# Optimization experiments

Hardware: AMD Instinct MI355X
Metric: run time of the kernel (lower is better)

## Reference

```python
import jax, jax.numpy as jnp
import numpy as np

D_MODEL = 512
NUM_HEADS = 8
HEAD_DIM = D_MODEL // NUM_HEADS


def setup_inputs() -> dict:
    key = jax.random.key(0)
    ks = jax.random.split(key, 12)
    B, S, D = 4, 2048, D_MODEL
    s = 1.0 / np.sqrt(D)
    return {
        "x": jax.random.normal(ks[0], (B, S, D), dtype=jnp.float32),
        "timestamps": jax.random.uniform(ks[1], (B, S), dtype=jnp.float32),
        "attention_mask": jnp.ones((B, S), dtype=jnp.int32),
        "Wq": jax.random.normal(ks[2], (D, D), dtype=jnp.float32) * s,
        "bq": jnp.zeros((D,), dtype=jnp.float32),
        "Wk": jax.random.normal(ks[3], (D, D), dtype=jnp.float32) * s,
        "bk": jnp.zeros((D,), dtype=jnp.float32),
        "Wv": jax.random.normal(ks[4], (D, D), dtype=jnp.float32) * s,
        "bv": jnp.zeros((D,), dtype=jnp.float32),
        "Wo": jax.random.normal(ks[5], (D, D), dtype=jnp.float32) * s,
        "bo": jnp.zeros((D,), dtype=jnp.float32),
        "decay_lambda": jnp.ones((NUM_HEADS,), dtype=jnp.float32),
    }


def reference(x, timestamps, attention_mask, Wq, bq, Wk, bk, Wv, bv, Wo, bo, decay_lambda):
    B, S, D = x.shape
    H, hd = NUM_HEADS, HEAD_DIM
    scale = hd ** -0.5
    q = (x @ Wq + bq).reshape(B, S, H, hd)
    k = (x @ Wk + bk).reshape(B, S, H, hd)
    v = (x @ Wv + bv).reshape(B, S, H, hd)
    # [B,H,S,S] raw scores
    scores = jnp.einsum("bihd,bjhd->bhij", q, k) * scale
    # learnable exponential time decay, multiplied into scores
    time_diff_abs = jnp.abs(timestamps[:, :, None] - timestamps[:, None, :])  # [B,S,S]
    lam = jax.nn.softplus(decay_lambda)  # [H]
    decay_bias = jnp.exp(-lam[None, :, None, None] * time_diff_abs[:, None])  # [B,H,S,S]
    scores = scores * decay_bias
    # mask over key positions
    scores = jnp.where(attention_mask[:, None, None, :] == 0, -jnp.inf, scores)
    attn = jax.nn.softmax(scores, axis=-1)
    out = jnp.einsum("bhij,bjhd->bihd", attn, v).reshape(B, S, D)
    out = out @ Wo + bo
    return out, attn
```

## Files before the change

kernel.cpp:

```cpp
#include <hip/hip_runtime.h>


#define S_LEN  2048
#define DM     512
#define NH     8
#define HDIM   64
#define BATCH  4
#define BHN    32
#define BSROWS 8192

typedef __attribute__((ext_vector_type(8))) short short8v;
typedef __attribute__((ext_vector_type(8))) unsigned short ushort8v;
typedef __attribute__((ext_vector_type(4))) unsigned short ushort4v;
typedef __attribute__((ext_vector_type(4))) float f32x4;
typedef __attribute__((ext_vector_type(2))) unsigned int uint2v;

static __device__ __forceinline__ unsigned short bf16_rne(float f){
  unsigned int u = __float_as_uint(f);
  u = (u + 0x7FFFu + ((u >> 16) & 1u)) >> 16;
  return (unsigned short)u;
}
static __device__ __forceinline__ float bf16_f32(unsigned short h){
  return __uint_as_float(((unsigned int)h) << 16);
}
static __device__ __forceinline__ unsigned int pack2bf(float a, float b){
  return (unsigned int)bf16_rne(a) | ((unsigned int)bf16_rne(b) << 16);
}
static __device__ __forceinline__ f32x4 mfma16(short8v a, short8v b, f32x4 c){
  return __builtin_amdgcn_mfma_f32_16x16x32_bf16(a, b, c, 0, 0, 0);
}
static __device__ __forceinline__ void gll16(const unsigned short* g, unsigned short* l){
  __builtin_amdgcn_global_load_lds(
      (const __attribute__((address_space(1))) unsigned int*)g,
      (__attribute__((address_space(3))) unsigned int*)l, 16, 0, 0);
}

__global__ void k_split(const float* __restrict__ src,
                        unsigned short* __restrict__ hi,
                        unsigned short* __restrict__ lo, int n){
  for (int i = blockIdx.x*blockDim.x + threadIdx.x; i < n;
       i += gridDim.x*blockDim.x){
    float f = src[i];
    unsigned short h = bf16_rne(f);
    hi[i] = h;
    lo[i] = bf16_rne(f - bf16_f32(h));
  }
}

__global__ void k_wsplit(const float* __restrict__ W,
                         unsigned short* __restrict__ Thi,
                         unsigned short* __restrict__ Tlo){
  int idx = blockIdx.x*blockDim.x + threadIdx.x;
  int n = idx >> 9, k = idx & 511;
  float f = W[k*DM + n];
  unsigned short h = bf16_rne(f);
  Thi[idx] = h;
  Tlo[idx] = bf16_rne(f - bf16_f32(h));
}

__global__ __launch_bounds__(256, 3) void k_gemm_split(
    const unsigned short* __restrict__ Ahi, const unsigned short* __restrict__ Alo,
    const unsigned short* __restrict__ BThi, const unsigned short* __restrict__ BTlo,
    const float* __restrict__ bias,
    float* __restrict__ outF,
    unsigned short* __restrict__ outHi, unsigned short* __restrict__ outLo,
    int M, int N, int K, int mode, float cscale)
{
  __shared__ __align__(16) unsigned short At[2][2][128][32];
  __shared__ __align__(16) unsigned short Bt[2][2][64][32];
  const int lane = threadIdx.x & 63, w = threadIdx.x >> 6;
  const int lr = lane & 15, lk = lane >> 4;
  const int rowbase = blockIdx.y*128;
  const int colbase = blockIdx.x*64;
  const int wrow = (w >> 1)*64;
  const int wcol = (w & 1)*32;

  const int srow = w*16 + (lane>>2);
  const int ssw  = ((lane&3) ^ ((lane>>3)&3))*8;
  const unsigned short* asrc_h = Ahi + (size_t)(rowbase + srow)*K + ssw;
  const unsigned short* asrc_l = Alo + (size_t)(rowbase + srow)*K + ssw;
  const unsigned short* bsrc_h = BThi + (size_t)(colbase + srow)*K + ssw;
  const unsigned short* bsrc_l = BTlo + (size_t)(colbase + srow)*K + ssw;
  unsigned short* adst_h = &At[0][0][w*16][0];
  unsigned short* adst_l = &At[0][1][w*16][0];
  unsigned short* bdst_h = &Bt[0][0][w*16][0];
  unsigned short* bdst_l = &Bt[0][1][w*16][0];

#define GSTAGE(KS, BB) { \
    int k0_ = (KS)*32; \
    gll16(asrc_h + k0_,              adst_h + (BB)*8192); \
    gll16(asrc_h + (size_t)64*K + k0_, adst_h + (BB)*8192 + 2048); \
    gll16(asrc_l + k0_,              adst_l + (BB)*8192); \
    gll16(asrc_l + (size_t)64*K + k0_, adst_l + (BB)*8192 + 2048); \
    gll16(bsrc_h + k0_,              bdst_h + (BB)*4096); \
    gll16(bsrc_l + k0_,              bdst_l + (BB)*4096); }

  const int csw = (lk ^ ((lr>>1)&3))*8;
  const unsigned short* Ard_h = &At[0][0][wrow + lr][0] + csw;
  const unsigned short* Ard_l = &At[0][1][wrow + lr][0] + csw;
  const unsigned short* Brd_h = &Bt[0][0][wcol + lr][0] + csw;
  const unsigned short* Brd_l = &Bt[0][1][wcol + lr][0] + csw;

  f32x4 acc[4][2];
#pragma unroll
  for (int mi=0; mi<4; ++mi)
#pragma unroll
    for (int ni=0; ni<2; ++ni) acc[mi][ni] = (f32x4){0.f,0.f,0.f,0.f};

  GSTAGE(0, 0);
  __syncthreads();

  const int NKS = K >> 5;
  for (int ks = 0; ks < NKS; ++ks){
    const int c = ks & 1;
    if (ks + 1 < NKS) GSTAGE(ks+1, c^1);
    short8v ah[4], al[4], bhf[2], blf[2];
#pragma unroll
    for (int mi=0; mi<4; ++mi){
      ah[mi] = *(const short8v*)(Ard_h + c*8192 + mi*512);
      al[mi] = *(const short8v*)(Ard_l + c*8192 + mi*512);
    }
#pragma unroll
    for (int ni=0; ni<2; ++ni){
      bhf[ni] = *(const short8v*)(Brd_h + c*4096 + ni*512);
      blf[ni] = *(const short8v*)(Brd_l + c*4096 + ni*512);
    }
#pragma unroll
    for (int mi=0; mi<4; ++mi)
#pragma unroll
      for (int ni=0; ni<2; ++ni){
        acc[mi][ni] = mfma16(ah[mi], blf[ni], acc[mi][ni]);
        acc[mi][ni] = mfma16(al[mi], bhf[ni], acc[mi][ni]);
        acc[mi][ni] = mfma16(ah[mi], bhf[ni], acc[mi][ni]);
      }
    __syncthreads();
  }
#undef GSTAGE

#pragma unroll
  for (int mi=0; mi<4; ++mi)
#pragma unroll
    for (int ni=0; ni<2; ++ni){
      const int col = colbase + wcol + ni*16 + lr;
      const int row0 = rowbase + wrow + mi*16 + lk*4;
      if (mode == 1){
        int b = row0 >> 11, s0 = row0 & 2047, hh = col >> 6, d = col & 63;
        ushort4v t;
#pragma unroll
        for (int r=0;r<4;++r)
          t[r] = bf16_rne((acc[mi][ni][r] + bias[col]) * cscale);
        *(ushort4v*)(outHi + ((size_t)(b*NH + hh)*HDIM + d)*S_LEN + s0) = t;
      } else {
#pragma unroll
        for (int r=0;r<4;++r){
          int row = row0 + r;
          float cvl = (acc[mi][ni][r] + bias[col]) * cscale;
          if (mode == 2){
            outF[(size_t)row*N + col] = cvl;
          } else {
            int b = row >> 11, s = row & 2047, hh = col >> 6, d = col & 63;
            size_t off = (((size_t)(b*NH + hh))*S_LEN + s)*HDIM + d;
            unsigned short hb = bf16_rne(cvl);
            outHi[off] = hb;
            outLo[off] = bf16_rne(cvl - bf16_f32(hb));
          }
        }
      }
    }
}

__global__ __launch_bounds__(256) void k_rowsum(
    const unsigned short* __restrict__ qhi,
    const unsigned short* __restrict__ khi,
    const float* __restrict__ ts, const int* __restrict__ am,
    const float* __restrict__ dlam,
    float* __restrict__ rs_part)
{
  __shared__ __align__(16) unsigned short K_t[2][32][64];
  __shared__ __align__(16) float ts_l[1024];
  __shared__ __align__(16) float mb_l[1024];
  const int w = threadIdx.x >> 6, lane = threadIdx.x & 63;
  const int lr = lane & 15, lk = lane >> 4;
  const int wg = blockIdx.x;
  const int sw = (wg & 7)*256 + (wg >> 3);
  const int bh = sw >> 6, rem = sw & 63, it = rem >> 1, jh = rem & 1;
  const int b = bh >> 3, h = bh & 7;
  const int i0 = it*64 + w*16;
  const int j0 = jh*1024;

  const float* tsb = ts + b*S_LEN;
  const int*   amb = am + b*S_LEN;
  for (int i = threadIdx.x; i < 1024; i += 256){
    ts_l[i] = tsb[j0+i];
    mb_l[i] = amb[j0+i] ? 0.f : -1e30f;
  }

  float nlam2 = -log1pf(expf(dlam[h])) * 1.44269504f;
  nlam2 = __uint_as_float(__builtin_amdgcn_readfirstlane(__float_as_uint(nlam2)));

  size_t qoff = ((size_t)bh*S_LEN + i0 + lr)*HDIM + lk*8;
  const short8v qh0 = *(const short8v*)(qhi + qoff);
  const short8v qh1 = *(const short8v*)(qhi + qoff + 32);
  const float ti = tsb[i0 + lr];

  const unsigned short* kbh = khi + ((size_t)bh*S_LEN + j0)*HDIM;
  const unsigned short* ksrc = kbh + ((lane>>3))*64
                             + (((lane&7)^((lane>>3)&7))*8) + w*512;
  unsigned short* kdst = &K_t[0][0][0] + w*512;

  gll16(ksrc, kdst);
  __syncthreads();

  float rs = 0.f;
  for (int t = 0; t < 32; ++t){
    const int c = t & 1;
    if (t < 31) gll16(ksrc + (t+1)*2048, kdst + (c^1)*2048);
#pragma unroll
    for (int s = 0; s < 2; ++s){
      const unsigned short* Kr = &K_t[c][s*16 + lr][0];
      short8v a0 = *(const short8v*)(Kr + ((lk ^ (lr&7))*8));
      short8v a1 = *(const short8v*)(Kr + (((4+lk) ^ (lr&7))*8));
      f32x4 sA = (f32x4){0.f,0.f,0.f,0.f};
      sA = mfma16(a0, qh0, sA);
      sA = mfma16(a1, qh1, sA);
      const int jb = t*32 + s*16 + lk*4;
      f32x4 ts4 = *(const f32x4*)&ts_l[jb];
      f32x4 mb4 = *(const f32x4*)&mb_l[jb];
#pragma unroll
      for (int r=0;r<4;++r){
        float dec = __builtin_amdgcn_exp2f(nlam2 * fabsf(ti - ts4[r]));
        rs += __builtin_amdgcn_exp2f(__builtin_fmaf(sA[r], dec, mb4[r]));
      }
    }
    __syncthreads();
  }
  rs += __shfl_xor(rs, 16, 64);
  rs += __shfl_xor(rs, 32, 64);
  if (lane < 16)
    rs_part[(size_t)(jh*BHN + bh)*S_LEN + i0 + lane] = rs;
}

__global__ __launch_bounds__(256, 4) void k_pass2(
    const unsigned short* __restrict__ qhi, const unsigned short* __restrict__ qlo,
    const unsigned short* __restrict__ khi, const unsigned short* __restrict__ klo,
    const unsigned short* __restrict__ vT,
    const float* __restrict__ ts, const int* __restrict__ am,
    const float* __restrict__ dlam,
    const float* __restrict__ rs_part,
    float* __restrict__ attn,
    unsigned short* __restrict__ p0hi, unsigned short* __restrict__ p0lo,
    unsigned short* __restrict__ p1hi, unsigned short* __restrict__ p1lo)
{
  __shared__ __align__(16) unsigned short K_t[2][2][32][64];
  __shared__ __align__(16) unsigned short V_t[2][64][32];
  __shared__ __align__(16) float ts_l[1024];
  __shared__ __align__(16) float mb_l[1024];
  __shared__ __align__(16) unsigned int pb[4][16][20];
  const int w = threadIdx.x >> 6, lane = threadIdx.x & 63;
  const int lr = lane & 15, lk = lane >> 4;
  const int wg = blockIdx.x;
  const int sw = (wg & 7)*256 + (wg >> 3);
  const int bh = sw >> 6, rem = sw & 63, it = rem >> 1, jh = rem & 1;
  const int b = bh >> 3, h = bh & 7;
  const int i0 = it*64 + w*16;
  const int j0 = jh*1024;

  const float* tsb = ts + b*S_LEN;
  const int*   amb = am + b*S_LEN;
  for (int i = threadIdx.x; i < 1024; i += 256){
    ts_l[i] = tsb[j0+i];
    mb_l[i] = amb[j0+i] ? 0.f : -1e30f;
  }

  float nlam2 = -log1pf(expf(dlam[h])) * 1.44269504f;
  nlam2 = __uint_as_float(__builtin_amdgcn_readfirstlane(__float_as_uint(nlam2)));

  size_t qoff = ((size_t)bh*S_LEN + i0 + lr)*HDIM + lk*8;
  const short8v qh0 = *(const short8v*)(qhi + qoff);
  const short8v qh1 = *(const short8v*)(qhi + qoff + 32);
  const short8v ql0 = *(const short8v*)(qlo + qoff);
  const short8v ql1 = *(const short8v*)(qlo + qoff + 32);
  const float ti = tsb[i0 + lr];

  float tot = rs_part[(size_t)bh*S_LEN + i0 + lr]
            + rs_part[(size_t)(BHN + bh)*S_LEN + i0 + lr];
  const float rinv = tot > 0.f ? 1.f/tot : 0.f;

  const unsigned short* kbh = khi + ((size_t)bh*S_LEN + j0)*HDIM;
  const unsigned short* kbl = klo + ((size_t)bh*S_LEN + j0)*HDIM;
  const unsigned short* vtb = vT + (size_t)bh*HDIM*S_LEN;
  unsigned int* pbw = &pb[w][0][0];

  const int ksw = ((lane&7)^((lane>>3)&7))*8;
  const unsigned short* ksrc_h = kbh + (lane>>3)*64 + ksw + w*512;
  const unsigned short* ksrc_l = kbl + (lane>>3)*64 + ksw + w*512;
  const unsigned short* vsrc = vtb + ((size_t)(w*16 + (lane>>2)))*S_LEN + j0
                             + (((lane&3)^((lane>>4)&3))*8);
  unsigned short* kdst_h = &K_t[0][0][0][0] + w*512;
  unsigned short* kdst_l = &K_t[0][1][0][0] + w*512;
  unsigned short* vdst   = &V_t[0][0][0]    + w*512;

  const unsigned int abase = (unsigned int)(bh*S_LEN + i0 + lr)*S_LEN + j0;

  gll16(ksrc_h, kdst_h);
  gll16(ksrc_l, kdst_l);
  gll16(vsrc,   vdst);
  __syncthreads();

  f32x4 oaccT0 = (f32x4){0.f,0.f,0.f,0.f};
  f32x4 oaccT1 = (f32x4){0.f,0.f,0.f,0.f};
  f32x4 oaccT2 = (f32x4){0.f,0.f,0.f,0.f};
  f32x4 oaccT3 = (f32x4){0.f,0.f,0.f,0.f};

  for (int t = 0; t < 32; ++t){
    const int c = t & 1;
    if (t < 31){
      gll16(ksrc_h + (t+1)*2048, kdst_h + (c^1)*4096);
      gll16(ksrc_l + (t+1)*2048, kdst_l + (c^1)*4096);
      gll16(vsrc   + (t+1)*32,   vdst   + (c^1)*2048);
    }
#pragma unroll
    for (int s = 0; s < 2; ++s){
      const unsigned short* Kr0 = &K_t[c][0][s*16 + lr][0];
      const unsigned short* Kr1 = &K_t[c][1][s*16 + lr][0];
      short8v kh0 = *(const short8v*)(Kr0 + ((lk ^ (lr&7))*8));
      short8v kh1 = *(const short8v*)(Kr0 + (((4+lk) ^ (lr&7))*8));
      short8v kl0 = *(const short8v*)(Kr1 + ((lk ^ (lr&7))*8));
      short8v kl1 = *(const short8v*)(Kr1 + (((4+lk) ^ (lr&7))*8));
      f32x4 s1 = (f32x4){0.f,0.f,0.f,0.f};
      s1 = mfma16(kh0, ql0, s1);
      s1 = mfma16(kl0, qh0, s1);
      s1 = mfma16(kh1, ql1, s1);
      s1 = mfma16(kl1, qh1, s1);
      f32x4 s2 = (f32x4){0.f,0.f,0.f,0.f};
      s2 = mfma16(kh0, qh0, s2);
      s2 = mfma16(kh1, qh1, s2);
      const int jb = t*32 + s*16 + lk*4;
      f32x4 ts4 = *(const f32x4*)&ts_l[jb];
      f32x4 mb4 = *(const f32x4*)&mb_l[jb];
      f32x4 pv;
#pragma unroll
      for (int r=0;r<4;++r){
        float sa = s1[r] + s2[r];
        float dec = __builtin_amdgcn_exp2f(nlam2 * fabsf(ti - ts4[r]));
        float e = __builtin_amdgcn_exp2f(__builtin_fmaf(sa, dec, mb4[r]));
        pv[r] = e * rinv;
      }
      *(f32x4*)(attn + abase + jb) = pv;
      uint2v pk; pk.x = pack2bf(pv[0], pv[1]); pk.y = pack2bf(pv[2], pv[3]);
      *(uint2v*)&pbw[lr*20 + s*8 + 2*lk] = pk;
    }
    short8v pa = *(const short8v*)&pbw[lr*20 + 4*lk];
    const int vsw = (lr>>2)&3;
    short8v vf0 = *(const short8v*)&V_t[c][ 0 + lr][(lk ^ vsw)*8];
    short8v vf1 = *(const short8v*)&V_t[c][16 + lr][(lk ^ vsw)*8];
    short8v vf2 = *(const short8v*)&V_t[c][32 + lr][(lk ^ vsw)*8];
    short8v vf3 = *(const short8v*)&V_t[c][48 + lr][(lk ^ vsw)*8];
    oaccT0 = mfma16(vf0, pa, oaccT0);
    oaccT1 = mfma16(vf1, pa, oaccT1);
    oaccT2 = mfma16(vf2, pa, oaccT2);
    oaccT3 = mfma16(vf3, pa, oaccT3);
    __syncthreads();
  }

  unsigned short* phi = jh ? p1hi : p0hi;
  unsigned short* plo = jh ? p1lo : p0lo;
  const size_t rowb = (size_t)(b*S_LEN + i0 + lr)*DM + h*HDIM + lk*4;
  float oa[4][4] = {
    {oaccT0[0],oaccT0[1],oaccT0[2],oaccT0[3]},
    {oaccT1[0],oaccT1[1],oaccT1[2],oaccT1[3]},
    {oaccT2[0],oaccT2[1],oaccT2[2],oaccT2[3]},
    {oaccT3[0],oaccT3[1],oaccT3[2],oaccT3[3]}};
#pragma unroll
  for (int nt=0;nt<4;++nt){
    ushort4v hh, ll;
#pragma unroll
    for (int r=0;r<4;++r){
      float vv = oa[nt][r];
      unsigned short hb = bf16_rne(vv);
      hh[r] = hb;
      ll[r] = bf16_rne(vv - bf16_f32(hb));
    }
    *(ushort4v*)(phi + rowb + nt*16) = hh;
    *(ushort4v*)(plo + rowb + nt*16) = ll;
  }
}

__global__ __launch_bounds__(256) void k_combine(
    const unsigned short* __restrict__ h1, const unsigned short* __restrict__ l1,
    unsigned short* __restrict__ oh, unsigned short* __restrict__ ol, int n8)
{
  int i = blockIdx.x*blockDim.x + threadIdx.x;
  if (i >= n8) return;
  size_t base = (size_t)i*8;
  ushort8v a = *(const ushort8v*)(oh + base);
  ushort8v bq = *(const ushort8v*)(ol + base);
  ushort8v c = *(const ushort8v*)(h1 + base);
  ushort8v d = *(const ushort8v*)(l1 + base);
  ushort8v rh, rl;
#pragma unroll
  for (int j=0;j<8;++j){
    float f = bf16_f32(a[j]) + bf16_f32(bq[j]) + bf16_f32(c[j]) + bf16_f32(d[j]);
    unsigned short hb = bf16_rne(f);
    rh[j] = hb;
    rl[j] = bf16_rne(f - bf16_f32(hb));
  }
  *(ushort8v*)(oh + base) = rh;
  *(ushort8v*)(ol + base) = rl;
}

extern "C" void kernel_launch(void* const* d_in, const int* in_sizes, int n_in,
                              void* d_out, int out_size, void* d_ws, size_t ws_size,
                              hipStream_t stream){
  const float* x  = (const float*)d_in[0];
  const float* ts = (const float*)d_in[1];
  const int*   am = (const int*)d_in[2];
  const float* Wq = (const float*)d_in[3];
  const float* bq = (const float*)d_in[4];
  const float* Wk = (const float*)d_in[5];
  const float* bk = (const float*)d_in[6];
  const float* Wv = (const float*)d_in[7];
  const float* bv = (const float*)d_in[8];
  const float* Wo = (const float*)d_in[9];
  const float* bo = (const float*)d_in[10];
  const float* dl = (const float*)d_in[11];

  char* ws = (char*)d_ws;
  unsigned short* xhi = (unsigned short*)(ws);
  unsigned short* xlo = (unsigned short*)(ws + 8388608ull);
  unsigned short* wqt_hi = (unsigned short*)(ws + 16777216ull + 0ull*524288ull);
  unsigned short* wqt_lo = (unsigned short*)(ws + 16777216ull + 1ull*524288ull);
  unsigned short* wkt_hi = (unsigned short*)(ws + 16777216ull + 2ull*524288ull);
  unsigned short* wkt_lo = (unsigned short*)(ws + 16777216ull + 3ull*524288ull);
  unsigned short* wvt_hi = (unsigned short*)(ws + 16777216ull + 4ull*524288ull);
  unsigned short* wvt_lo = (unsigned short*)(ws + 16777216ull + 5ull*524288ull);
  unsigned short* wot_hi = (unsigned short*)(ws + 16777216ull + 6ull*524288ull);
  unsigned short* wot_lo = (unsigned short*)(ws + 16777216ull + 7ull*524288ull);
  unsigned short* qhi = (unsigned short*)(ws + 20971520ull + 0ull*8388608ull);
  unsigned short* qlo = (unsigned short*)(ws + 20971520ull + 1ull*8388608ull);
  unsigned short* khi = (unsigned short*)(ws + 20971520ull + 2ull*8388608ull);
  unsigned short* klo = (unsigned short*)(ws + 20971520ull + 3ull*8388608ull);
  unsigned short* vt  = (unsigned short*)(ws + 20971520ull + 4ull*8388608ull);
  float* rs_part = (float*)(ws + 16777216ull);

  float* outp  = (float*)d_out;
  float* attnp = outp + (size_t)BSROWS*DM;
  unsigned short* p1hi = (unsigned short*)d_out;
  unsigned short* p1lo = p1hi + 4194304ull;

  k_split<<<4096, 256, 0, stream>>>(x, xhi, xlo, BSROWS*DM);
  k_wsplit<<<1024, 256, 0, stream>>>(Wq, wqt_hi, wqt_lo);
  k_wsplit<<<1024, 256, 0, stream>>>(Wk, wkt_hi, wkt_lo);
  k_wsplit<<<1024, 256, 0, stream>>>(Wv, wvt_hi, wvt_lo);
  k_wsplit<<<1024, 256, 0, stream>>>(Wo, wot_hi, wot_lo);

  dim3 pg(DM/64, BSROWS/128);
  k_gemm_split<<<pg, 256, 0, stream>>>(xhi, xlo, wqt_hi, wqt_lo, bq,
                                       nullptr, qhi, qlo, BSROWS, DM, DM, 0,
                                       0.18033688f);
  k_gemm_split<<<pg, 256, 0, stream>>>(xhi, xlo, wkt_hi, wkt_lo, bk,
                                       nullptr, khi, klo, BSROWS, DM, DM, 0, 1.f);
  k_gemm_split<<<pg, 256, 0, stream>>>(xhi, xlo, wvt_hi, wvt_lo, bv,
                                       nullptr, vt, nullptr, BSROWS, DM, DM, 1, 1.f);

  k_rowsum<<<2048, 256, 0, stream>>>(qhi, khi, ts, am, dl, rs_part);
  k_pass2<<<2048, 256, 0, stream>>>(qhi, qlo, khi, klo, vt, ts, am, dl,
                                    rs_part, attnp, xhi, xlo, p1hi, p1lo);
  k_combine<<<2048, 256, 0, stream>>>(p1hi, p1lo, xhi, xlo, 524288);
  k_gemm_split<<<pg, 256, 0, stream>>>(xhi, xlo, wot_hi, wot_lo, bo,
                                       outp, nullptr, nullptr, BSROWS, DM, DM, 2, 1.f);

  (void)in_sizes; (void)n_in; (void)out_size; (void)ws_size;
}
```

Baseline: 399.6 us.

## Widen projection GEMM tile to 128x128 and fuse weight-split launches

The split-bf16 GEMM block tile grows from 128x64 to 128x128, so each wave computes a 64x64 sub-tile with a 4x4 accumulator array. The staging loads and LDS B-buffer are resized to match, and the occupancy hint is dropped from the launch bounds. This raises reuse of the A operand per LDS load and halves the block count, at the cost of higher register and LDS use per block. Separately, the four weight transpose/split kernels are merged into one launch to cut launch overhead.

New measurement: 418.6 us. 4.7% more time.

```diff
diff --git a/kernel.cpp b/kernel.cpp
--- a/kernel.cpp
+++ b/kernel.cpp
@@ -47,18 +47,28 @@
   }
 }
 
-__global__ void k_wsplit(const float* __restrict__ W,
-                         unsigned short* __restrict__ Thi,
-                         unsigned short* __restrict__ Tlo){
+__global__ void k_wsplit4(
+    const float* __restrict__ Wq, const float* __restrict__ Wk,
+    const float* __restrict__ Wv, const float* __restrict__ Wo,
+    unsigned short* __restrict__ qh, unsigned short* __restrict__ ql,
+    unsigned short* __restrict__ kh, unsigned short* __restrict__ kl,
+    unsigned short* __restrict__ vh, unsigned short* __restrict__ vl,
+    unsigned short* __restrict__ oh, unsigned short* __restrict__ ol)
+{
   int idx = blockIdx.x*blockDim.x + threadIdx.x;
-  int n = idx >> 9, k = idx & 511;
+  int wsel = idx >> 18;
+  int off  = idx & 262143;
+  int n = off >> 9, k = off & 511;
+  const float* W = wsel==0 ? Wq : wsel==1 ? Wk : wsel==2 ? Wv : Wo;
+  unsigned short* H = wsel==0 ? qh : wsel==1 ? kh : wsel==2 ? vh : oh;
+  unsigned short* L = wsel==0 ? ql : wsel==1 ? kl : wsel==2 ? vl : ol;
   float f = W[k*DM + n];
   unsigned short h = bf16_rne(f);
-  Thi[idx] = h;
-  Tlo[idx] = bf16_rne(f - bf16_f32(h));
-}
-
-__global__ __launch_bounds__(256, 3) void k_gemm_split(
+  H[off] = h;
+  L[off] = bf16_rne(f - bf16_f32(h));
+}
+
+__global__ __launch_bounds__(256) void k_gemm_split(
     const unsigned short* __restrict__ Ahi, const unsigned short* __restrict__ Alo,
     const unsigned short* __restrict__ BThi, const unsigned short* __restrict__ BTlo,
     const float* __restrict__ bias,
@@ -67,33 +77,35 @@
     int M, int N, int K, int mode, float cscale)
 {
   __shared__ __align__(16) unsigned short At[2][2][128][32];
-  __shared__ __align__(16) unsigned short Bt[2][2][64][32];
+  __shared__ __align__(16) unsigned short Bt[2][2][128][32];
   const int lane = threadIdx.x & 63, w = threadIdx.x >> 6;
   const int lr = lane & 15, lk = lane >> 4;
   const int rowbase = blockIdx.y*128;
-  const int colbase = blockIdx.x*64;
+  const int colbase = blockIdx.x*128;
   const int wrow = (w >> 1)*64;
-  const int wcol = (w & 1)*32;
-
-  const int srow = w*16 + (lane>>2);
+  const int wcol = (w & 1)*64;
+
+  const int srow = w*32 + (lane>>2);
   const int ssw  = ((lane&3) ^ ((lane>>3)&3))*8;
-  const unsigned short* asrc_h = Ahi + (size_t)(rowbase + srow)*K + ssw;
-  const unsigned short* asrc_l = Alo + (size_t)(rowbase + srow)*K + ssw;
+  const unsigned short* asrc_h = Ahi  + (size_t)(rowbase + srow)*K + ssw;
+  const unsigned short* asrc_l = Alo  + (size_t)(rowbase + srow)*K + ssw;
   const unsigned short* bsrc_h = BThi + (size_t)(colbase + srow)*K + ssw;
   const unsigned short* bsrc_l = BTlo + (size_t)(colbase + srow)*K + ssw;
-  unsigned short* adst_h = &At[0][0][w*16][0];
-  unsigned short* adst_l = &At[0][1][w*16][0];
-  unsigned short* bdst_h = &Bt[0][0][w*16][0];
-  unsigned short* bdst_l = &Bt[0][1][w*16][0];
+  unsigned short* adst_h = &At[0][0][w*32][0];
+  unsigned short* adst_l = &At[0][1][w*32][0];
+  unsigned short* bdst_h = &Bt[0][0][w*32][0];
+  unsigned short* bdst_l = &Bt[0][1][w*32][0];
 
 #define GSTAGE(KS, BB) { \
     int k0_ = (KS)*32; \
-    gll16(asrc_h + k0_,              adst_h + (BB)*8192); \
-    gll16(asrc_h + (size_t)64*K + k0_, adst_h + (BB)*8192 + 2048); \
-    gll16(asrc_l + k0_,              adst_l + (BB)*8192); \
-    gll16(asrc_l + (size_t)64*K + k0_, adst_l + (BB)*8192 + 2048); \
-    gll16(bsrc_h + k0_,              bdst_h + (BB)*4096); \
-    gll16(bsrc_l + k0_,              bdst_l + (BB)*4096); }
+    gll16(asrc_h + k0_,                adst_h + (BB)*8192); \
+    gll16(asrc_h + (size_t)16*K + k0_, adst_h + (BB)*8192 + 512); \
+    gll16(asrc_l + k0_,                adst_l + (BB)*8192); \
+    gll16(asrc_l + (size_t)16*K + k0_, adst_l + (BB)*8192 + 512); \
+    gll16(bsrc_h + k0_,                bdst_h + (BB)*8192); \
+    gll16(bsrc_h + (size_t)16*K + k0_, bdst_h + (BB)*8192 + 512); \
+    gll16(bsrc_l + k0_,                bdst_l + (BB)*8192); \
+    gll16(bsrc_l + (size_t)16*K + k0_, bdst_l + (BB)*8192 + 512); }
 
   const int csw = (lk ^ ((lr>>1)&3))*8;
   const unsigned short* Ard_h = &At[0][0][wrow + lr][0] + csw;
@@ -101,11 +113,11 @@
   const unsigned short* Brd_h = &Bt[0][0][wcol + lr][0] + csw;
   const unsigned short* Brd_l = &Bt[0][1][wcol + lr][0] + csw;
 
-  f32x4 acc[4][2];
+  f32x4 acc[4][4];
 #pragma unroll
   for (int mi=0; mi<4; ++mi)
 #pragma unroll
-    for (int ni=0; ni<2; ++ni) acc[mi][ni] = (f32x4){0.f,0.f,0.f,0.f};
+    for (int ni=0; ni<4; ++ni) acc[mi][ni] = (f32x4){0.f,0.f,0.f,0.f};
 
   GSTAGE(0, 0);
   __syncthreads();
@@ -114,21 +126,21 @@
   for (int ks = 0; ks < NKS; ++ks){
     const int c = ks & 1;
     if (ks + 1 < NKS) GSTAGE(ks+1, c^1);
-    short8v ah[4], al[4], bhf[2], blf[2];
+    short8v ah[4], al[4], bhf[4], blf[4];
 #pragma unroll
     for (int mi=0; mi<4; ++mi){
       ah[mi] = *(const short8v*)(Ard_h + c*8192 + mi*512);
       al[mi] = *(const short8v*)(Ard_l + c*8192 + mi*512);
     }
 #pragma unroll
-    for (int ni=0; ni<2; ++ni){
-      bhf[ni] = *(const short8v*)(Brd_h + c*4096 + ni*512);
-      blf[ni] = *(const short8v*)(Brd_l + c*4096 + ni*512);
+    for (int ni=0; ni<4; ++ni){
+      bhf[ni] = *(const short8v*)(Brd_h + c*8192 + ni*512);
+      blf[ni] = *(const short8v*)(Brd_l + c*8192 + ni*512);
     }
 #pragma unroll
     for (int mi=0; mi<4; ++mi)
 #pragma unroll
-      for (int ni=0; ni<2; ++ni){
+      for (int ni=0; ni<4; ++ni){
         acc[mi][ni] = mfma16(ah[mi], blf[ni], acc[mi][ni]);
         acc[mi][ni] = mfma16(al[mi], bhf[ni], acc[mi][ni]);
         acc[mi][ni] = mfma16(ah[mi], bhf[ni], acc[mi][ni]);
@@ -140,7 +152,7 @@
 #pragma unroll
   for (int mi=0; mi<4; ++mi)
 #pragma unroll
-    for (int ni=0; ni<2; ++ni){
+    for (int ni=0; ni<4; ++ni){
       const int col = colbase + wcol + ni*16 + lr;
       const int row0 = rowbase + wrow + mi*16 + lk*4;
       if (mode == 1){
@@ -449,12 +461,11 @@
   unsigned short* p1lo = p1hi + 4194304ull;
 
   k_split<<<4096, 256, 0, stream>>>(x, xhi, xlo, BSROWS*DM);
-  k_wsplit<<<1024, 256, 0, stream>>>(Wq, wqt_hi, wqt_lo);
-  k_wsplit<<<1024, 256, 0, stream>>>(Wk, wkt_hi, wkt_lo);
-  k_wsplit<<<1024, 256, 0, stream>>>(Wv, wvt_hi, wvt_lo);
-  k_wsplit<<<1024, 256, 0, stream>>>(Wo, wot_hi, wot_lo);
-
-  dim3 pg(DM/64, BSROWS/128);
+  k_wsplit4<<<4096, 256, 0, stream>>>(Wq, Wk, Wv, Wo,
+                                      wqt_hi, wqt_lo, wkt_hi, wkt_lo,
+                                      wvt_hi, wvt_lo, wot_hi, wot_lo);
+
+  dim3 pg(DM/128, BSROWS/128);
   k_gemm_split<<<pg, 256, 0, stream>>>(xhi, xlo, wqt_hi, wqt_lo, bq,
                                        nullptr, qhi, qlo, BSROWS, DM, DM, 0,
                                        0.18033688f);
```
